# Performance work log

Hardware: AMD Instinct MI355X
Metric: run time of the kernel (lower is better)

The kernel has to match this reference:

```python
import jax, jax.numpy as jnp
import numpy as np

H8, W8 = 64, 64
H4, W4 = 128, 128
C_LAT, C_HI = 256, 128
N_Q = 1024
ORIG_H, ORIG_W = 512, 512
NUM_ITERS = 4
TEMP = 20.0
DIM = 4 + C_HI + C_LAT        # 388 mixer output dim
IN_DIM = DIM + 3 * 49         # 535 mixer input dim
HID = 512


def _unit(v):
    return v / jnp.sqrt(jnp.maximum(jnp.sum(v * v, axis=-1, keepdims=True), 1e-12))


def setup_inputs() -> dict:
    key = jax.random.key(0)
    ks = jax.random.split(key, 20)
    fg = _unit(jax.random.normal(ks[0], (1, H8, W8, C_LAT), jnp.float32))
    hg = _unit(jax.random.normal(ks[1], (1, H4, W4, C_HI), jnp.float32))
    qf = _unit(jax.random.normal(ks[2], (1, N_Q, C_LAT), jnp.float32))
    hq = _unit(jax.random.normal(ks[3], (1, N_Q, C_HI), jnp.float32))
    p = lambda k, s, sc=0.05: sc * jax.random.normal(k, s, jnp.float32)
    return dict(
        feature_grid=fg, hires_feats_grid=hg, query_feats=qf, hires_query_feats=hq,
        hid1_w=p(ks[4], (16, 1, 3, 3)), hid1_b=jnp.zeros((16,), jnp.float32),
        hid2_w=p(ks[5], (1, 16, 3, 3)), hid2_b=jnp.zeros((1,), jnp.float32),
        hid3_w=p(ks[6], (32, 16, 3, 3)), hid3_b=jnp.zeros((32,), jnp.float32),
        hid4_w=p(ks[7], (32, 16)), hid4_b=jnp.zeros((16,), jnp.float32),
        occ_w=p(ks[8], (16, 2)), occ_b=jnp.zeros((2,), jnp.float32),
        mix_in_w=p(ks[9], (IN_DIM, HID), 0.02), mix_in_b=jnp.zeros((HID,), jnp.float32),
        mix_out_w=p(ks[10], (HID, DIM), 0.02), mix_out_b=jnp.zeros((DIM,), jnp.float32),
    )


def _conv2d(x, w, b, stride, pad):
    y = jax.lax.conv_general_dilated(x, w, (stride, stride), pad,
                                     dimension_numbers=('NCHW', 'OIHW', 'NCHW'))
    return y + b[None, :, None, None]


def _bilinear_sample(grid, coords):
    # grid [H,W,C]; coords [..., 2] as (y, x); edge-clamped bilinear gather.
    H, W = grid.shape[0], grid.shape[1]
    y, x = coords[..., 0], coords[..., 1]
    y0f, x0f = jnp.floor(y), jnp.floor(x)
    wy, wx = (y - y0f)[..., None], (x - x0f)[..., None]
    y0 = jnp.clip(y0f.astype(jnp.int32), 0, H - 1)
    y1 = jnp.clip(y0f.astype(jnp.int32) + 1, 0, H - 1)
    x0 = jnp.clip(x0f.astype(jnp.int32), 0, W - 1)
    x1 = jnp.clip(x0f.astype(jnp.int32) + 1, 0, W - 1)
    g00, g01 = grid[y0, x0], grid[y0, x1]
    g10, g11 = grid[y1, x0], grid[y1, x1]
    return (g00 * (1 - wy) * (1 - wx) + g01 * (1 - wy) * wx
            + g10 * wy * (1 - wx) + g11 * wy * wx)


def _forward(fg, hg, qf, hq, hid1_w, hid1_b, hid2_w, hid2_b, hid3_w, hid3_b,
             hid4_w, hid4_b, occ_w, occ_b, mix_in_w, mix_in_b, mix_out_w, mix_out_b):
    # --- tracks_from_cost_volume ---
    cv = jnp.einsum('bnc,bhwc->bnhw', qf, fg)                 # [1,N,64,64]
    b, n, h, w = cv.shape
    x = cv.reshape(b * n, 1, h, w)
    occ_map = jax.nn.relu(_conv2d(x, hid1_w, hid1_b, 1, 'SAME'))   # [bn,16,h,w]
    pmap = _conv2d(occ_map, hid2_w, hid2_b, 1, 'SAME').reshape(b * n, h * w)
    heat = jax.nn.softmax(pmap * TEMP, axis=-1).reshape(b * n, h, w)
    ey = jnp.einsum('bhw,h->b', heat, jnp.arange(h, dtype=jnp.float32))
    ex = jnp.einsum('bhw,w->b', heat, jnp.arange(w, dtype=jnp.float32))
    points = jnp.stack([ex * (ORIG_W / w), ey * (ORIG_H / h)], -1).reshape(b, n, 2)
    op = jnp.pad(occ_map, ((0, 0), (0, 0), (0, 2), (0, 2)))
    o3 = jax.nn.relu(_conv2d(op, hid3_w, hid3_b, 2, 'VALID'))
    o3 = o3.mean((-1, -2))                                     # [bn,32]
    o3 = jax.nn.relu(o3 @ hid4_w + hid4_b)
    o3 = (o3 @ occ_w + occ_b).reshape(b, n, 2)
    occ, expd = o3[..., 0], o3[..., 1]

    # --- iterative pips refinement ---
    cy, cx = jnp.meshgrid(jnp.arange(-3, 4), jnp.arange(-3, 4), indexing='ij')
    ctx = jnp.stack([cy, cx], -1).reshape(-1, 2).astype(jnp.float32)   # [49,2] (dy,dx)
    fg_avg = fg.reshape(1, H8 // 2, 2, W8 // 2, 2, C_LAT).mean((2, 4))
    pyramid = [hg, fg, fg_avg]
    feats = jnp.concatenate([hq, qf], -1)                      # [1,N,384]
    pos = points
    for it in range(NUM_ITERS):
        if it == 0:
            queries = [hq[0], qf[0], qf[0]]
        else:
            queries = [feats[0, :, :C_HI], feats[0, :, C_HI:], feats[0, :, C_HI:]]
        corrs = []
        for grid, q in zip(pyramid, queries):
            gh, gw = grid.shape[1], grid.shape[2]
            scale = jnp.array([gw / ORIG_W, gh / ORIG_H], jnp.float32)
            c = (pos[0] * scale)[:, ::-1]                      # (x,y)->(y,x), [N,2]
            coords2 = c[:, None, :] + ctx[None]                # [N,49,2]
            nb = _bilinear_sample(grid[0], coords2)            # [N,49,C]
            corrs.append(jnp.einsum('nsc,nc->ns', nb, q))
        corrs = jnp.concatenate(corrs, -1)[None]               # [1,N,147]
        mlp_in = jnp.concatenate([jnp.zeros_like(pos), occ[..., None],
                                  expd[..., None], feats, corrs], -1)
        res = jax.nn.gelu(mlp_in @ mix_in_w + mix_in_b) @ mix_out_w + mix_out_b
        pos = pos + res[..., :2]
        occ = occ + res[..., 2]
        expd = expd + res[..., 3]
        feats = feats + res[..., 4:]
    return jnp.concatenate([pos, occ[..., None], expd[..., None]], -1)  # [1,N,4]


def reference(feature_grid, hires_feats_grid, query_feats, hires_query_feats,
              hid1_w, hid1_b, hid2_w, hid2_b, hid3_w, hid3_b, hid4_w, hid4_b,
              occ_w, occ_b, mix_in_w, mix_in_b, mix_out_w, mix_out_b):
    return _forward(feature_grid, hires_feats_grid, query_feats, hires_query_feats,
                    hid1_w, hid1_b, hid2_w, hid2_b, hid3_w, hid3_b, hid4_w, hid4_b,
                    occ_w, occ_b, mix_in_w, mix_in_b, mix_out_w, mix_out_b)
```

## Files before the change

### kernel.cpp

```cpp
#include <hip/hip_runtime.h>
#include <hip/hip_bf16.h>
#include <math.h>


#define NQ 1024
#define TEMPF 20.0f
#define DIMV 388
#define INDIM 535
#define KPAD 544
#define HID 512

#define WS_CVB     0
#define WS_WIT     2097152
#define WS_WOT     2236416
#define WS_FG16    2351104
#define WS_HG16    2875392
#define WS_AV16    3923968
#define WS_FGAVG   4194304
#define WS_POS     (WS_FGAVG + 262144)
#define WS_OCC     (WS_POS + NQ*2)
#define WS_EXPD    (WS_OCC + NQ)
#define WS_FEATS   (WS_EXPD + NQ)
#define WS_MLPIN   (WS_FEATS + NQ*384)
#define WS_HIDDEN  (WS_MLPIN + NQ*KPAD)
#define WS_W3B     (WS_HIDDEN + NQ*HID)
#define WS_PART    (WS_MLPIN + 278528)
#define WS_SUM3    WS_HIDDEN

#define OP 72
#define CVP 68

typedef __attribute__((ext_vector_type(8))) short bf16x8;
typedef __attribute__((ext_vector_type(4))) float f32x4;

union BU8 { uint4 u; __hip_bfloat16 h[8]; };

__global__ __launch_bounds__(256) void k_prep_cv(
    const float* __restrict__ fg, const float* __restrict__ qf,
    const float* __restrict__ hq, const float* __restrict__ w3,
    float* __restrict__ ws) {
  __shared__ __hip_bfloat16 A_s[32 * 32];
  __shared__ __hip_bfloat16 B_s[64 * 32];
  const int bx = blockIdx.x;
  const int t = threadIdx.x;

  if (bx >= 2048) {
    int i = (bx - 2048) * 256 + t;
    if (i < 262144) {
      int c = i & 255, ox = (i >> 8) & 31, oy = i >> 13;
      const float* b = fg + (((oy * 2) * 64 + ox * 2) << 8) + c;
      ws[WS_FGAVG + i] = 0.25f * (b[0] + b[256] + b[16384] + b[16384 + 256]);
    } else if (i < 262144 + 393216) {
      int j = i - 262144;
      int n = j / 384, c = j - n * 384;
      float v = (c < 128) ? hq[n * 128 + c] : qf[n * 256 + c - 128];
      ws[WS_FEATS + j] = v;
      __hip_bfloat16* mi = (__hip_bfloat16*)(ws + WS_MLPIN);
      mi[n * KPAD + 4 + c] = __float2bfloat16(v);
      if (c == 0) {
        mi[n * KPAD + 0] = __float2bfloat16(0.f);
        mi[n * KPAD + 1] = __float2bfloat16(0.f);
      }
    } else if (i < 262144 + 393216 + 5120) {
      int j = i - (262144 + 393216);
      int e = j & 7, qd = (j >> 3) & 3, nl = (j >> 5) & 15;
      int nt = (j >> 9) & 1, kt = j >> 10;
      int k = kt * 32 + qd * 8 + e;
      int ic = k & 15, tap = k >> 4;
      int oc = nt * 16 + nl;
      float v = (tap < 9) ? w3[(oc * 16 + ic) * 9 + tap] : 0.f;
      ((__hip_bfloat16*)(ws + WS_W3B))[j] = __float2bfloat16(v);
    } else if (i < 262144 + 393216 + 5120 + 524288) {
      int j = i - (262144 + 393216 + 5120);
      ws[WS_SUM3 + j] = 0.f;
    }
    return;
  }

  const int wv = t >> 6, lane = t & 63;
  const int wm = wv & 1, wn = wv >> 1;
  const int quad = lane >> 4, nl = lane & 15;
  const int p0 = (bx & 63) * 64, m0 = (bx >> 6) * 32;
  f32x4 acc0 = {0.f, 0.f, 0.f, 0.f};
  f32x4 acc1 = {0.f, 0.f, 0.f, 0.f};

  for (int k0 = 0; k0 < 256; k0 += 32) {
    {
      int r = t >> 3, c = t & 7;
      float4 v = *(const float4*)&qf[(m0 + r) * 256 + k0 + c * 4];
      union { __hip_bfloat16 h[4]; uint2 u; } pk;
      pk.h[0] = __float2bfloat16(v.x); pk.h[1] = __float2bfloat16(v.y);
      pk.h[2] = __float2bfloat16(v.z); pk.h[3] = __float2bfloat16(v.w);
      *(uint2*)&A_s[r * 32 + c * 4] = pk.u;
    }
    {
      int r = t >> 2, c = t & 3;
      const float* src = &fg[(p0 + r) * 256 + k0 + c * 8];
      float4 v0 = *(const float4*)src;
      float4 v1 = *(const float4*)(src + 4);
      union { __hip_bfloat16 h[8]; uint4 u; } pk;
      pk.h[0] = __float2bfloat16(v0.x); pk.h[1] = __float2bfloat16(v0.y);
      pk.h[2] = __float2bfloat16(v0.z); pk.h[3] = __float2bfloat16(v0.w);
      pk.h[4] = __float2bfloat16(v1.x); pk.h[5] = __float2bfloat16(v1.y);
      pk.h[6] = __float2bfloat16(v1.z); pk.h[7] = __float2bfloat16(v1.w);
      *(uint4*)&B_s[r * 32 + c * 8] = pk.u;
    }
    __syncthreads();
    bf16x8 a = *(const bf16x8*)&A_s[(16 * wm + nl) * 32 + quad * 8];
    bf16x8 b0 = *(const bf16x8*)&B_s[(32 * wn + nl) * 32 + quad * 8];
    bf16x8 b1 = *(const bf16x8*)&B_s[(32 * wn + 16 + nl) * 32 + quad * 8];
    acc0 = __builtin_amdgcn_mfma_f32_16x16x32_bf16(a, b0, acc0, 0, 0, 0);
    acc1 = __builtin_amdgcn_mfma_f32_16x16x32_bf16(a, b1, acc1, 0, 0, 0);
    __syncthreads();
  }
  __hip_bfloat16* cvb = (__hip_bfloat16*)ws;
#pragma unroll
  for (int nt = 0; nt < 2; nt++) {
    int n = p0 + 32 * wn + nt * 16 + nl;
#pragma unroll
    for (int r = 0; r < 4; r++) {
      int m = m0 + 16 * wm + quad * 4 + r;
      cvb[m * 4096 + n] = __float2bfloat16(nt ? acc1[r] : acc0[r]);
    }
  }
}

__global__ __launch_bounds__(256, 5) void k_head_stripe(
    const float* __restrict__ h1w, const float* __restrict__ h1b,
    const float* __restrict__ h2w, const float* __restrict__ h2b,
    const float* __restrict__ h3b, float* __restrict__ ws) {
  __shared__ float cvs[8 * CVP];
  __shared__ float occ[6 * 16 * OP];

  const int bx = blockIdx.x;
  const int q = bx >> 4, st = bx & 15;
  const int y0 = st * 4;
  const int t = threadIdx.x;
  const int wv = t >> 6, lane = t & 63;
  const int role = (wv + bx) & 3;
  const __hip_bfloat16* cvb = (const __hip_bfloat16*)ws + q * 4096;

  if (t < 192) {
    int rc = t >> 1, side = t & 1;
    *(float4*)&occ[rc * OP + side * 68] = make_float4(0.f, 0.f, 0.f, 0.f);
  }
  if (st == 0 || st == 15) {
    int r = (st == 0) ? 0 : 5;
    for (int i = t; i < 16 * 18; i += 256)
      *(float4*)&occ[(r * 16 + (i / 18)) * OP + (i % 18) * 4] =
          make_float4(0.f, 0.f, 0.f, 0.f);
  }
#pragma unroll
  for (int j = 0; j < 2; j++) {
    int i = t + 256 * j;
    int lr = i >> 6, x = i & 63;
    int g = y0 - 2 + lr;
    cvs[lr * CVP + x + 1] =
        (g >= 0 && g < 64) ? __bfloat162float(cvb[g * 64 + x]) : 0.f;
  }
  if (t < 32) {
    int rr = t >> 2, c = t & 3;
    cvs[rr * CVP + ((c == 0) ? 0 : (64 + c))] = 0.f;
  }
  __syncthreads();

  {
    const int x = lane;
    const int chg = wv * 4;
    float w1r[4][9], b1r[4];
#pragma unroll
    for (int k = 0; k < 4; k++) {
      b1r[k] = h1b[chg + k];
#pragma unroll
      for (int j = 0; j < 9; j++) w1r[k][j] = h1w[(chg + k) * 9 + j];
    }
    float win[3][3];
#pragma unroll
    for (int j = 0; j < 3; j++) {
      const float* cp = &cvs[j * CVP + x];
      win[j][0] = cp[0]; win[j][1] = cp[1]; win[j][2] = cp[2];
    }
    for (int r = 0; r < 6; r++) {
      if (r > 0) {
#pragma unroll
        for (int c = 0; c < 3; c++) { win[0][c] = win[1][c]; win[1][c] = win[2][c]; }
        const float* cp = &cvs[(r + 2) * CVP + x];
        win[2][0] = cp[0]; win[2][1] = cp[1]; win[2][2] = cp[2];
      }
      int yo = y0 - 1 + r;
      if (yo >= 0 && yo <= 63) {
#pragma unroll
        for (int k = 0; k < 4; k++) {
          float a = b1r[k];
#pragma unroll
          for (int ky = 0; ky < 3; ky++)
            a += w1r[k][3 * ky] * win[ky][0] + w1r[k][3 * ky + 1] * win[ky][1] +
                 w1r[k][3 * ky + 2] * win[ky][2];
          occ[(r * 16 + chg + k) * OP + x + 4] = fmaxf(a, 0.f);
        }
      }
    }
  }
  __syncthreads();

  if (role == 1 || role == 2) {
    const __hip_bfloat16* W3B = (const __hip_bfloat16*)(ws + WS_W3B);
    const int oyl = role - 1;
    const int nl = lane & 15;
    const int qd = lane >> 4, qh = qd >> 1, ql = qd & 1;
    f32x4 acc00 = {0.f,0.f,0.f,0.f}, acc01 = {0.f,0.f,0.f,0.f};
    f32x4 acc10 = {0.f,0.f,0.f,0.f}, acc11 = {0.f,0.f,0.f,0.f};
#pragma unroll
    for (int kt = 0; kt < 5; kt++) {
      int tap = kt * 2 + qh;
      int tv = (tap < 9) ? tap : 0;
      int ky = (tv >= 6) ? 2 : ((tv >= 3) ? 1 : 0);
      int kx = tv - 3 * ky;
      const float* ap =
          &occ[((2 * oyl + 1 + ky) * 16 + ql * 8) * OP + 4 + kx + 2 * nl];
      union { bf16x8 v; __hip_bfloat16 h[8]; } a0u, a1u;
      if (tap < 9) {
#pragma unroll
        for (int j = 0; j < 8; j++) {
          a0u.h[j] = __float2bfloat16(ap[j * OP]);
          a1u.h[j] = __float2bfloat16(ap[j * OP + 32]);
        }
      } else {
#pragma unroll
        for (int j = 0; j < 8; j++) {
          a0u.h[j] = __float2bfloat16(0.f);
          a1u.h[j] = __float2bfloat16(0.f);
        }
      }
      bf16x8 b0 = *(const bf16x8*)&W3B[((kt * 2 + 0) * 16 + nl) * 32 + qd * 8];
      bf16x8 b1 = *(const bf16x8*)&W3B[((kt * 2 + 1) * 16 + nl) * 32 + qd * 8];
      acc00 = __builtin_amdgcn_mfma_f32_16x16x32_bf16(a0u.v, b0, acc00, 0, 0, 0);
      acc01 = __builtin_amdgcn_mfma_f32_16x16x32_bf16(a0u.v, b1, acc01, 0, 0, 0);
      acc10 = __builtin_amdgcn_mfma_f32_16x16x32_bf16(a1u.v, b0, acc10, 0, 0, 0);
      acc11 = __builtin_amdgcn_mfma_f32_16x16x32_bf16(a1u.v, b1, acc11, 0, 0, 0);
    }
    float bb0 = h3b[nl], bb1 = h3b[16 + nl];
    float s0 = 0.f, s1 = 0.f;
#pragma unroll
    for (int r = 0; r < 4; r++) {
      s0 += fmaxf(acc00[r] + bb0, 0.f) + fmaxf(acc10[r] + bb0, 0.f);
      s1 += fmaxf(acc01[r] + bb1, 0.f) + fmaxf(acc11[r] + bb1, 0.f);
    }
    s0 += __shfl_xor(s0, 16); s0 += __shfl_xor(s0, 32);
    s1 += __shfl_xor(s1, 16); s1 += __shfl_xor(s1, 32);
    if (lane < 16) {
      atomicAdd(&ws[WS_SUM3 + (q * 16 + st) * 32 + nl], s0);
      atomicAdd(&ws[WS_SUM3 + (q * 16 + st) * 32 + 16 + nl], s1);
    }
  } else {
    const int rl = ((role == 3) ? 2 : 0) + (lane >> 5);
    const int yg = y0 + rl;
    const int x0 = (lane & 31) * 2;
    float pa = 0.f, pb = 0.f;
    for (int ch = 0; ch < 16; ch++) {
#pragma unroll
      for (int ky = 0; ky < 3; ky++) {
        const float* bp = &occ[((rl + ky) * 16 + ch) * OP + x0];
        float f0 = bp[3];
        float2 fm = *(const float2*)(bp + 4);
        float f3 = bp[6];
        float wa = h2w[ch * 9 + 3 * ky], wb = h2w[ch * 9 + 3 * ky + 1],
              wc = h2w[ch * 9 + 3 * ky + 2];
        pa += wa * f0 + wb * fm.x + wc * fm.y;
        pb += wa * fm.x + wb * fm.y + wc * f3;
      }
    }
    float bb = h2b[0];
    float v0 = (pa + bb) * TEMPF, v1 = (pb + bb) * TEMPF;
    float mg = fmaxf(v0, v1);
#pragma unroll
    for (int off = 1; off < 64; off <<= 1) mg = fmaxf(mg, __shfl_xor(mg, off));
    float e0 = __expf(v0 - mg), e1 = __expf(v1 - mg);
    float s = e0 + e1;
    float sx = e0 * (float)x0 + e1 * (float)(x0 + 1);
    float sy = s * (float)yg;
#pragma unroll
    for (int off = 1; off < 64; off <<= 1) {
      s += __shfl_xor(s, off);
      sx += __shfl_xor(sx, off);
      sy += __shfl_xor(sy, off);
    }
    if (lane == 0) {
      int slot = q * 32 + st * 2 + ((role == 3) ? 1 : 0);
      *(float4*)&ws[WS_PART + slot * 4] = make_float4(mg, s, sx, sy);
    }
  }
}

__global__ __launch_bounds__(256) void k_merge_cvt(
    const float* __restrict__ w4, const float* __restrict__ b4,
    const float* __restrict__ w5, const float* __restrict__ b5,
    const float* __restrict__ wi, const float* __restrict__ wo,
    const float* __restrict__ fg, const float* __restrict__ hg,
    float* __restrict__ ws) {
  {
    int i = blockIdx.x * 256 + threadIdx.x;
    __hip_bfloat16* WIT = (__hip_bfloat16*)(ws + WS_WIT);
    __hip_bfloat16* WOT = (__hip_bfloat16*)(ws + WS_WOT);
    if (i < 278528) {
      int n = i / KPAD, k = i - n * KPAD;
      float v = (k < INDIM) ? wi[k * HID + n] : 0.f;
      WIT[i] = __float2bfloat16(v);
    } else if (i < 507904) {
      int j = i - 278528;
      int n = j >> 9, k = j & 511;
      float v = (n < DIMV) ? wo[k * DIMV + n] : 0.f;
      WOT[j] = __float2bfloat16(v);
    } else {
      int j = i - 507904;
      if (j < 1048576) {
        ((__hip_bfloat16*)(ws + WS_FG16))[j] = __float2bfloat16(fg[j]);
      } else if (j < 3145728) {
        int k = j - 1048576;
        ((__hip_bfloat16*)(ws + WS_HG16))[k] = __float2bfloat16(hg[k]);
      } else if (j < 3407872) {
        int k = j - 3145728;
        ((__hip_bfloat16*)(ws + WS_AV16))[k] = __float2bfloat16(ws[WS_FGAVG + k]);
      }
    }
  }
  if (blockIdx.x >= 256) return;

  __shared__ float sums_s[4][32];
  __shared__ float o4s[4][16];
  int t = threadIdx.x, wv = t >> 6, lane = t & 63;
  int q = blockIdx.x * 4 + wv;

  float M = -1e30f, S = 0.f, SX = 0.f, SY = 0.f;
  if (lane < 32) {
    float4 pv = *(const float4*)&ws[WS_PART + (q * 32 + lane) * 4];
    M = pv.x; S = pv.y; SX = pv.z; SY = pv.w;
  }
#pragma unroll
  for (int off = 1; off < 64; off <<= 1) {
    float Mo = __shfl_xor(M, off), So = __shfl_xor(S, off);
    float SXo = __shfl_xor(SX, off), SYo = __shfl_xor(SY, off);
    float Mn = fmaxf(M, Mo);
    float c1 = __expf(M - Mn), c2 = __expf(Mo - Mn);
    S = S * c1 + So * c2; SX = SX * c1 + SXo * c2; SY = SY * c1 + SYo * c2;
    M = Mn;
  }
  if (lane == 0) {
    ws[WS_POS + q * 2 + 0] = (SX / S) * 8.0f;
    ws[WS_POS + q * 2 + 1] = (SY / S) * 8.0f;
  }

  int ch = lane & 31, half = lane >> 5;
  float sm = 0.f;
#pragma unroll
  for (int s8 = 0; s8 < 8; s8++)
    sm += ws[WS_SUM3 + (q * 16 + half * 8 + s8) * 32 + ch];
  sm += __shfl_xor(sm, 32);
  if (lane < 32) sums_s[wv][lane] = sm * (1.f / 1024.f);
  __syncthreads();
  if (lane < 16) {
    float a = b4[lane];
#pragma unroll
    for (int i = 0; i < 32; i++) a += sums_s[wv][i] * w4[i * 16 + lane];
    o4s[wv][lane] = fmaxf(a, 0.f);
  }
  __syncthreads();
  if (lane < 2) {
    float r = b5[lane];
#pragma unroll
    for (int j = 0; j < 16; j++) r += o4s[wv][j] * w5[j * 2 + lane];
    __hip_bfloat16* mi = (__hip_bfloat16*)(ws + WS_MLPIN);
    if (lane == 0) { ws[WS_OCC + q] = r;  mi[q * KPAD + 2] = __float2bfloat16(r); }
    else           { ws[WS_EXPD + q] = r; mi[q * KPAD + 3] = __float2bfloat16(r); }
  }
}

__global__ __launch_bounds__(256) void k_corr(float* __restrict__ ws) {
  __shared__ float qs[384];
  __shared__ float dbuf[3][64];
  int t = threadIdx.x;
  int wv = t >> 6, lane = t & 63;
  int cl = lane & 15, sub = lane >> 4;
  int n = blockIdx.x;
  const float* feats = ws + WS_FEATS + n * 384;
  float posx = ws[WS_POS + n * 2 + 0];
  float posy = ws[WS_POS + n * 2 + 1];
  __hip_bfloat16* mi = (__hip_bfloat16*)(ws + WS_MLPIN) + n * KPAD;

  for (int col = t; col < 384; col += 256) qs[col] = feats[col];
  __syncthreads();

  float qh[8], qq[16];
#pragma unroll
  for (int j = 0; j < 8; j++) qh[j] = qs[cl * 8 + j];
#pragma unroll
  for (int j = 0; j < 16; j++) qq[j] = qs[128 + cl * 16 + j];

  const __hip_bfloat16* G0 = (const __hip_bfloat16*)(ws + WS_HG16);
  const __hip_bfloat16* G1 = (const __hip_bfloat16*)(ws + WS_FG16);
  const __hip_bfloat16* G2 = (const __hip_bfloat16*)(ws + WS_AV16);

#pragma unroll
  for (int L = 0; L < 3; L++) {
    const __hip_bfloat16* grid;
    int Hg, Wg;
    float scl;
    if (L == 0)      { grid = G0; Hg = 128; Wg = 128; scl = 0.25f; }
    else if (L == 1) { grid = G1; Hg = 64;  Wg = 64;  scl = 0.125f; }
    else             { grid = G2; Hg = 32;  Wg = 32;  scl = 0.0625f; }
    float cy = posy * scl, cx = posx * scl;
    int iy = (int)floorf(cy), ix = (int)floorf(cx);
#pragma unroll
    for (int g = 0; g < 4; g++) {
      int p = wv * 16 + g * 4 + sub;
      int a = p >> 3, b = p & 7;
      int row = iy + a - 3; row = row < 0 ? 0 : (row > Hg - 1 ? Hg - 1 : row);
      int col = ix + b - 3; col = col < 0 ? 0 : (col > Wg - 1 ? Wg - 1 : col);
      float acc = 0.f;
      if (L == 0) {
        BU8 g0; g0.u = *(const uint4*)(grid + (row * Wg + col) * 128 + cl * 8);
#pragma unroll
        for (int j = 0; j < 8; j++) acc += __bfloat162float(g0.h[j]) * qh[j];
      } else {
        const __hip_bfloat16* gp = grid + (row * Wg + col) * 256 + cl * 16;
        BU8 g0, g1;
        g0.u = *(const uint4*)gp;
        g1.u = *(const uint4*)(gp + 8);
#pragma unroll
        for (int j = 0; j < 8; j++) {
          acc += __bfloat162float(g0.h[j]) * qq[j];
          acc += __bfloat162float(g1.h[j]) * qq[8 + j];
        }
      }
      acc += __shfl_xor(acc, 1);
      acc += __shfl_xor(acc, 2);
      acc += __shfl_xor(acc, 4);
      acc += __shfl_xor(acc, 8);
      if (cl == 0) dbuf[L][p] = acc;
    }
  }
  __syncthreads();

  if (t < 147) {
    int L = t / 49, s = t - L * 49;
    int sa = s / 7, sb = s - sa * 7;
    float scl = (L == 0) ? 0.25f : ((L == 1) ? 0.125f : 0.0625f);
    float cy = posy * scl, cx = posx * scl;
    float wy = cy - floorf(cy), wx = cx - floorf(cx);
    int i00 = sa * 8 + sb;
    float d00 = dbuf[L][i00], d01 = dbuf[L][i00 + 1];
    float d10 = dbuf[L][i00 + 8], d11 = dbuf[L][i00 + 9];
    float corr = (1.f - wy) * (1.f - wx) * d00 + (1.f - wy) * wx * d01 +
                 wy * (1.f - wx) * d10 + wy * wx * d11;
    mi[388 + t] = __float2bfloat16(corr);
  }
}

__device__ __forceinline__ float gelu_tanh(float x) {
  float z = 0.7978845608028654f * (x + 0.044715f * x * x * x);
  z = fminf(fmaxf(z, -15.f), 15.f);
  float e = __expf(2.f * z);
  float th = (e - 1.f) / (e + 1.f);
  return 0.5f * x * (1.f + th);
}

__global__ __launch_bounds__(256) void k_mix1(
    const float* __restrict__ bias, float* __restrict__ ws) {
  __shared__ __hip_bfloat16 A_s[32 * 32];
  __shared__ __hip_bfloat16 B_s[32 * 32];
  const int t = threadIdx.x;
  const int wv = t >> 6, lane = t & 63;
  const int wm = wv & 1, wn = wv >> 1;
  const int quad = lane >> 4, nl = lane & 15;
  const int n0 = blockIdx.x * 32, m0 = blockIdx.y * 32;
  const unsigned short* Abf = (const unsigned short*)(ws + WS_MLPIN);
  const unsigned short* WIT = (const unsigned short*)(ws + WS_WIT);
  f32x4 acc = {0.f, 0.f, 0.f, 0.f};

  for (int k0 = 0; k0 < KPAD; k0 += 32) {
    if (t < 128) {
      int r = t >> 2, c = t & 3;
      *(uint4*)&A_s[r * 32 + c * 8] =
          *(const uint4*)&Abf[(m0 + r) * KPAD + k0 + c * 8];
    } else {
      int tt = t - 128;
      int r = tt >> 2, c = tt & 3;
      *(uint4*)&B_s[r * 32 + c * 8] =
          *(const uint4*)&WIT[(n0 + r) * KPAD + k0 + c * 8];
    }
    __syncthreads();
    bf16x8 a = *(const bf16x8*)&A_s[(16 * wm + nl) * 32 + quad * 8];
    bf16x8 b = *(const bf16x8*)&B_s[(16 * wn + nl) * 32 + quad * 8];
    acc = __builtin_amdgcn_mfma_f32_16x16x32_bf16(a, b, acc, 0, 0, 0);
    __syncthreads();
  }

  __hip_bfloat16* Hd = (__hip_bfloat16*)(ws + WS_HIDDEN);
  int nn = n0 + 16 * wn + nl;
  float bv = bias[nn];
#pragma unroll
  for (int r = 0; r < 4; r++) {
    int m = m0 + 16 * wm + quad * 4 + r;
    Hd[m * HID + nn] = __float2bfloat16(gelu_tanh(acc[r] + bv));
  }
}

__global__ __launch_bounds__(256) void k_mix2(
    const float* __restrict__ bias, float* __restrict__ ws,
    float* __restrict__ out) {
  __shared__ __hip_bfloat16 A_s[32 * 32];
  __shared__ __hip_bfloat16 B_s[32 * 32];
  const int t = threadIdx.x;
  const int wv = t >> 6, lane = t & 63;
  const int wm = wv & 1, wn = wv >> 1;
  const int quad = lane >> 4, nl = lane & 15;
  const int n0 = blockIdx.x * 32, m0 = blockIdx.y * 32;
  const unsigned short* Abf = (const unsigned short*)(ws + WS_HIDDEN);
  const unsigned short* WOT = (const unsigned short*)(ws + WS_WOT);
  f32x4 acc = {0.f, 0.f, 0.f, 0.f};

  for (int k0 = 0; k0 < HID; k0 += 32) {
    if (t < 128) {
      int r = t >> 2, c = t & 3;
      *(uint4*)&A_s[r * 32 + c * 8] =
          *(const uint4*)&Abf[(m0 + r) * HID + k0 + c * 8];
    } else {
      int tt = t - 128;
      int r = tt >> 2, c = tt & 3;
      *(uint4*)&B_s[r * 32 + c * 8] =
          *(const uint4*)&WOT[(n0 + r) * HID + k0 + c * 8];
    }
    __syncthreads();
    bf16x8 a = *(const bf16x8*)&A_s[(16 * wm + nl) * 32 + quad * 8];
    bf16x8 b = *(const bf16x8*)&B_s[(16 * wn + nl) * 32 + quad * 8];
    acc = __builtin_amdgcn_mfma_f32_16x16x32_bf16(a, b, acc, 0, 0, 0);
    __syncthreads();
  }

  int col = n0 + 16 * wn + nl;
  if (col < DIMV) {
    float bv = bias[col];
    __hip_bfloat16* mib = (__hip_bfloat16*)(ws + WS_MLPIN);
#pragma unroll
    for (int r = 0; r < 4; r++) {
      int m = m0 + 16 * wm + quad * 4 + r;
      float rr = acc[r] + bv;
      if (col < 2) {
        float v = ws[WS_POS + m * 2 + col] + rr;
        ws[WS_POS + m * 2 + col] = v;
        out[m * 4 + col] = v;
      } else if (col == 2) {
        float v = ws[WS_OCC + m] + rr;
        ws[WS_OCC + m] = v;
        out[m * 4 + 2] = v;
        mib[m * KPAD + 2] = __float2bfloat16(v);
      } else if (col == 3) {
        float v = ws[WS_EXPD + m] + rr;
        ws[WS_EXPD + m] = v;
        out[m * 4 + 3] = v;
        mib[m * KPAD + 3] = __float2bfloat16(v);
      } else {
        float v = ws[WS_FEATS + m * 384 + (col - 4)] + rr;
        ws[WS_FEATS + m * 384 + (col - 4)] = v;
        mib[m * KPAD + col] = __float2bfloat16(v);
      }
    }
  }
}

extern "C" void kernel_launch(void* const* d_in, const int* in_sizes, int n_in,
                              void* d_out, int out_size, void* d_ws, size_t ws_size,
                              hipStream_t stream) {
  const float* fg = (const float*)d_in[0];
  const float* hg = (const float*)d_in[1];
  const float* qf = (const float*)d_in[2];
  const float* hq = (const float*)d_in[3];
  const float* w1 = (const float*)d_in[4];
  const float* b1 = (const float*)d_in[5];
  const float* w2 = (const float*)d_in[6];
  const float* b2 = (const float*)d_in[7];
  const float* w3 = (const float*)d_in[8];
  const float* b3 = (const float*)d_in[9];
  const float* w4 = (const float*)d_in[10];
  const float* b4 = (const float*)d_in[11];
  const float* w5 = (const float*)d_in[12];
  const float* b5 = (const float*)d_in[13];
  const float* wi = (const float*)d_in[14];
  const float* bi = (const float*)d_in[15];
  const float* wo = (const float*)d_in[16];
  const float* bo = (const float*)d_in[17];
  float* ws = (float*)d_ws;
  float* out = (float*)d_out;

  k_prep_cv<<<6676, 256, 0, stream>>>(fg, qf, hq, w3, ws);
  k_head_stripe<<<16384, 256, 0, stream>>>(w1, b1, w2, b2, b3, ws);
  k_merge_cvt<<<15296, 256, 0, stream>>>(w4, b4, w5, b5, wi, wo, fg, hg, ws);
  for (int it = 0; it < 4; it++) {
    k_corr<<<1024, 256, 0, stream>>>(ws);
    k_mix1<<<dim3(16, 32), 256, 0, stream>>>(bi, ws);
    k_mix2<<<dim3(13, 32), 256, 0, stream>>>(bo, ws, out);
  }
}
```

Before: 314.8 us.

## Fuse hid2 conv into hid1 pass and store occupancy as swizzled bf16

The hid1 conv loop now also accumulates the hid2 3x3 conv partial sums in registers. Neighbours are combined through lane shuffles and the per-wave partials go through a small shared buffer, so the second pass over all 16 channels goes away. The shared occupancy tile is now stored as bf16 in a channel-innermost layout with an XOR swizzle, so the MFMA A-fragments load as single 16-byte vectors instead of 8 strided scalar converts. W3 B-fragments are preloaded into registers before the barrier. Fixed wave roles replace the rotating role assignment, and launch bounds drop from 5 to 4 blocks, which adds register pressure.

```diff
diff --git a/kernel.cpp b/kernel.cpp
--- a/kernel.cpp
+++ b/kernel.cpp
@@ -27,13 +27,19 @@
 #define WS_PART    (WS_MLPIN + 278528)
 #define WS_SUM3    WS_HIDDEN
 
-#define OP 72
 #define CVP 68
+#define ROWP 2368
 
 typedef __attribute__((ext_vector_type(8))) short bf16x8;
 typedef __attribute__((ext_vector_type(4))) float f32x4;
 
 union BU8 { uint4 u; __hip_bfloat16 h[8]; };
+
+__device__ __forceinline__ int occ_off(int r, int idx, int c) {
+  int o = idx * 32 + c * 2;
+  o ^= ((idx >> 2) & 3) << 4;
+  return r * ROWP + o;
+}
 
 __global__ __launch_bounds__(256) void k_prep_cv(
     const float* __restrict__ fg, const float* __restrict__ qf,
@@ -125,30 +131,31 @@
   }
 }
 
-__global__ __launch_bounds__(256, 5) void k_head_stripe(
+__global__ __launch_bounds__(256, 4) void k_head_stripe(
     const float* __restrict__ h1w, const float* __restrict__ h1b,
     const float* __restrict__ h2w, const float* __restrict__ h2b,
     const float* __restrict__ h3b, float* __restrict__ ws) {
   __shared__ float cvs[8 * CVP];
-  __shared__ float occ[6 * 16 * OP];
+  __shared__ float4 occ_t4[6 * ROWP / 16];
+  __shared__ float pmbuf[4][4][64];
+  char* occ_t = (char*)occ_t4;
 
   const int bx = blockIdx.x;
   const int q = bx >> 4, st = bx & 15;
   const int y0 = st * 4;
   const int t = threadIdx.x;
   const int wv = t >> 6, lane = t & 63;
-  const int role = (wv + bx) & 3;
   const __hip_bfloat16* cvb = (const __hip_bfloat16*)ws + q * 4096;
 
   if (t < 192) {
-    int rc = t >> 1, side = t & 1;
-    *(float4*)&occ[rc * OP + side * 68] = make_float4(0.f, 0.f, 0.f, 0.f);
+    int r = t >> 5, j = t & 31;
+    int off = r * ROWP + ((j < 16) ? j * 8 : 2176 + (j - 16) * 8);
+    *(uint2*)(occ_t + off) = make_uint2(0u, 0u);
   }
   if (st == 0 || st == 15) {
     int r = (st == 0) ? 0 : 5;
-    for (int i = t; i < 16 * 18; i += 256)
-      *(float4*)&occ[(r * 16 + (i / 18)) * OP + (i % 18) * 4] =
-          make_float4(0.f, 0.f, 0.f, 0.f);
+    for (int i = t; i < 288; i += 256)
+      *(uint2*)(occ_t + r * ROWP + i * 8) = make_uint2(0u, 0u);
   }
 #pragma unroll
   for (int j = 0; j < 2; j++) {
@@ -164,15 +171,20 @@
   }
   __syncthreads();
 
+  const int x = lane;
+  const int chg = wv * 4;
+  float pm[4][3] = {{0.f, 0.f, 0.f}, {0.f, 0.f, 0.f},
+                    {0.f, 0.f, 0.f}, {0.f, 0.f, 0.f}};
   {
-    const int x = lane;
-    const int chg = wv * 4;
-    float w1r[4][9], b1r[4];
+    float w1r[4][9], b1r[4], w2r[4][9];
 #pragma unroll
     for (int k = 0; k < 4; k++) {
       b1r[k] = h1b[chg + k];
 #pragma unroll
-      for (int j = 0; j < 9; j++) w1r[k][j] = h1w[(chg + k) * 9 + j];
+      for (int j = 0; j < 9; j++) {
+        w1r[k][j] = h1w[(chg + k) * 9 + j];
+        w2r[k][j] = h2w[(chg + k) * 9 + j];
+      }
     }
     float win[3][3];
 #pragma unroll
@@ -180,6 +192,7 @@
       const float* cp = &cvs[j * CVP + x];
       win[j][0] = cp[0]; win[j][1] = cp[1]; win[j][2] = cp[2];
     }
+#pragma unroll
     for (int r = 0; r < 6; r++) {
       if (r > 0) {
 #pragma unroll
@@ -189,6 +202,7 @@
       }
       int yo = y0 - 1 + r;
       if (yo >= 0 && yo <= 63) {
+        union { __hip_bfloat16 h[4]; uint2 u; } pk;
 #pragma unroll
         for (int k = 0; k < 4; k++) {
           float a = b1r[k];
@@ -196,48 +210,65 @@
           for (int ky = 0; ky < 3; ky++)
             a += w1r[k][3 * ky] * win[ky][0] + w1r[k][3 * ky + 1] * win[ky][1] +
                  w1r[k][3 * ky + 2] * win[ky][2];
-          occ[(r * 16 + chg + k) * OP + x + 4] = fmaxf(a, 0.f);
+          a = fmaxf(a, 0.f);
+          pk.h[k] = __float2bfloat16(a);
+#pragma unroll
+          for (int ky = 0; ky < 3; ky++) {
+            int pr = r - ky;
+            if (pr >= 0 && pr <= 3) {
+              pm[pr][2] += a * w2r[k][3 * ky + 0];
+              pm[pr][1] += a * w2r[k][3 * ky + 1];
+              pm[pr][0] += a * w2r[k][3 * ky + 2];
+            }
+          }
         }
-      }
-    }
+        *(uint2*)(occ_t + occ_off(r, x + 4, chg)) = pk.u;
+      }
+    }
+  }
+#pragma unroll
+  for (int pr = 0; pr < 4; pr++) {
+    float lf = __shfl(pm[pr][2], lane - 1);
+    float rt = __shfl(pm[pr][0], lane + 1);
+    if (lane == 0) lf = 0.f;
+    if (lane == 63) rt = 0.f;
+    pmbuf[wv][pr][x] = pm[pr][1] + lf + rt;
+  }
+
+  const int nl = lane & 15;
+  const int qd = lane >> 4, qh = qd >> 1, ql = qd & 1;
+  bf16x8 bfr[10];
+  if (wv == 1 || wv == 2) {
+    const __hip_bfloat16* W3B = (const __hip_bfloat16*)(ws + WS_W3B);
+#pragma unroll
+    for (int s = 0; s < 10; s++)
+      bfr[s] = *(const bf16x8*)&W3B[(s * 16 + nl) * 32 + qd * 8];
   }
   __syncthreads();
 
-  if (role == 1 || role == 2) {
-    const __hip_bfloat16* W3B = (const __hip_bfloat16*)(ws + WS_W3B);
-    const int oyl = role - 1;
-    const int nl = lane & 15;
-    const int qd = lane >> 4, qh = qd >> 1, ql = qd & 1;
-    f32x4 acc00 = {0.f,0.f,0.f,0.f}, acc01 = {0.f,0.f,0.f,0.f};
-    f32x4 acc10 = {0.f,0.f,0.f,0.f}, acc11 = {0.f,0.f,0.f,0.f};
+  if (wv == 1 || wv == 2) {
+    const int oyl = wv - 1;
+    f32x4 acc00 = {0.f, 0.f, 0.f, 0.f}, acc01 = {0.f, 0.f, 0.f, 0.f};
+    f32x4 acc10 = {0.f, 0.f, 0.f, 0.f}, acc11 = {0.f, 0.f, 0.f, 0.f};
 #pragma unroll
     for (int kt = 0; kt < 5; kt++) {
       int tap = kt * 2 + qh;
-      int tv = (tap < 9) ? tap : 0;
-      int ky = (tv >= 6) ? 2 : ((tv >= 3) ? 1 : 0);
-      int kx = tv - 3 * ky;
-      const float* ap =
-          &occ[((2 * oyl + 1 + ky) * 16 + ql * 8) * OP + 4 + kx + 2 * nl];
-      union { bf16x8 v; __hip_bfloat16 h[8]; } a0u, a1u;
+      bf16x8 a0, a1;
       if (tap < 9) {
-#pragma unroll
-        for (int j = 0; j < 8; j++) {
-          a0u.h[j] = __float2bfloat16(ap[j * OP]);
-          a1u.h[j] = __float2bfloat16(ap[j * OP + 32]);
-        }
+        int ky = (tap >= 6) ? 2 : ((tap >= 3) ? 1 : 0);
+        int kx = tap - 3 * ky;
+        int R = 2 * oyl + 1 + ky;
+        int idx0 = 4 + kx + 2 * nl;
+        a0 = *(const bf16x8*)(occ_t + occ_off(R, idx0, ql * 8));
+        a1 = *(const bf16x8*)(occ_t + occ_off(R, idx0 + 32, ql * 8));
       } else {
-#pragma unroll
-        for (int j = 0; j < 8; j++) {
-          a0u.h[j] = __float2bfloat16(0.f);
-          a1u.h[j] = __float2bfloat16(0.f);
-        }
-      }
-      bf16x8 b0 = *(const bf16x8*)&W3B[((kt * 2 + 0) * 16 + nl) * 32 + qd * 8];
-      bf16x8 b1 = *(const bf16x8*)&W3B[((kt * 2 + 1) * 16 + nl) * 32 + qd * 8];
-      acc00 = __builtin_amdgcn_mfma_f32_16x16x32_bf16(a0u.v, b0, acc00, 0, 0, 0);
-      acc01 = __builtin_amdgcn_mfma_f32_16x16x32_bf16(a0u.v, b1, acc01, 0, 0, 0);
-      acc10 = __builtin_amdgcn_mfma_f32_16x16x32_bf16(a1u.v, b0, acc10, 0, 0, 0);
-      acc11 = __builtin_amdgcn_mfma_f32_16x16x32_bf16(a1u.v, b1, acc11, 0, 0, 0);
+        a0 = (bf16x8){0, 0, 0, 0, 0, 0, 0, 0};
+        a1 = a0;
+      }
+      acc00 = __builtin_amdgcn_mfma_f32_16x16x32_bf16(a0, bfr[2 * kt], acc00, 0, 0, 0);
+      acc01 = __builtin_amdgcn_mfma_f32_16x16x32_bf16(a0, bfr[2 * kt + 1], acc01, 0, 0, 0);
+      acc10 = __builtin_amdgcn_mfma_f32_16x16x32_bf16(a1, bfr[2 * kt], acc10, 0, 0, 0);
+      acc11 = __builtin_amdgcn_mfma_f32_16x16x32_bf16(a1, bfr[2 * kt + 1], acc11, 0, 0, 0);
     }
     float bb0 = h3b[nl], bb1 = h3b[16 + nl];
     float s0 = 0.f, s1 = 0.f;
@@ -253,32 +284,23 @@
       atomicAdd(&ws[WS_SUM3 + (q * 16 + st) * 32 + 16 + nl], s1);
     }
   } else {
-    const int rl = ((role == 3) ? 2 : 0) + (lane >> 5);
-    const int yg = y0 + rl;
+    const int rl = ((wv == 3) ? 2 : 0) + (lane >> 5);
     const int x0 = (lane & 31) * 2;
-    float pa = 0.f, pb = 0.f;
-    for (int ch = 0; ch < 16; ch++) {
-#pragma unroll
-      for (int ky = 0; ky < 3; ky++) {
-        const float* bp = &occ[((rl + ky) * 16 + ch) * OP + x0];
-        float f0 = bp[3];
-        float2 fm = *(const float2*)(bp + 4);
-        float f3 = bp[6];
-        float wa = h2w[ch * 9 + 3 * ky], wb = h2w[ch * 9 + 3 * ky + 1],
-              wc = h2w[ch * 9 + 3 * ky + 2];
-        pa += wa * f0 + wb * fm.x + wc * fm.y;
-        pb += wa * fm.x + wb * fm.y + wc * f3;
-      }
+    float sa = 0.f, sb = 0.f;
+#pragma unroll
+    for (int w = 0; w < 4; w++) {
+      float2 v = *(const float2*)&pmbuf[w][rl][x0];
+      sa += v.x; sb += v.y;
     }
     float bb = h2b[0];
-    float v0 = (pa + bb) * TEMPF, v1 = (pb + bb) * TEMPF;
+    float v0 = (sa + bb) * TEMPF, v1 = (sb + bb) * TEMPF;
     float mg = fmaxf(v0, v1);
 #pragma unroll
     for (int off = 1; off < 64; off <<= 1) mg = fmaxf(mg, __shfl_xor(mg, off));
     float e0 = __expf(v0 - mg), e1 = __expf(v1 - mg);
     float s = e0 + e1;
     float sx = e0 * (float)x0 + e1 * (float)(x0 + 1);
-    float sy = s * (float)yg;
+    float sy = s * (float)(y0 + rl);
 #pragma unroll
     for (int off = 1; off < 64; off <<= 1) {
       s += __shfl_xor(s, off);
@@ -286,7 +308,7 @@
       sy += __shfl_xor(sy, off);
     }
     if (lane == 0) {
-      int slot = q * 32 + st * 2 + ((role == 3) ? 1 : 0);
+      int slot = q * 32 + st * 2 + ((wv == 3) ? 1 : 0);
       *(float4*)&ws[WS_PART + slot * 4] = make_float4(mg, s, sx, sy);
     }
   }
```

After: 385.8 us. +22.6%, slower.
